# Kernel optimization log

Measured on AMD Instinct MI355X. Metric: run time of the kernel, lower is better.

The kernel has to match this reference:

```python
import jax, jax.numpy as jnp
import numpy as np

EPS = 1e-5  # torch BatchNorm1d default

def _bn(z, g, b):
    # training-mode BatchNorm1d: per-feature batch mean, biased variance
    m = jnp.mean(z, axis=0)
    v = jnp.mean((z - m) ** 2, axis=0)
    return (z - m) * jax.lax.rsqrt(v + EPS) * g + b

def _cell(x, h, c, Wx, Wh, gx, bx, gh, bh):
    gates = _bn(x @ Wx.T, gx, bx) + _bn(h @ Wh.T, gh, bh)  # [B, 4H]
    f, i, o, g = jnp.split(gates, 4, axis=1)  # chunk order f,i,o,g
    c2 = jax.nn.sigmoid(f) * c + jax.nn.sigmoid(i) * jnp.tanh(g)
    h2 = jax.nn.sigmoid(o) * jnp.tanh(c2)
    return h2, c2

def setup_inputs() -> dict:
    key = jax.random.key(0)
    B, H, OUT = 16384, 512, 256
    IN0 = 257  # input_size - 1 (x_dim 256 + y_dim 1)
    ks = jax.random.split(key, 16)
    def lin(k, fo, fi):
        s = 1.0 / np.sqrt(fi)
        return jax.random.uniform(k, (fo, fi), jnp.float32, -s, s)
    return {
        "x": jax.random.normal(ks[0], (B, 256), jnp.float32),
        "y": jax.random.normal(ks[1], (B, 1), jnp.float32),
        "h0": jax.random.normal(ks[2], (2, B, H), jnp.float32),
        "c0": jax.random.normal(ks[3], (2, B, H), jnp.float32),
        "Wx0": lin(ks[4], 4 * H, IN0),
        "Wh0": lin(ks[5], 4 * H, H),
        "gx0": jnp.ones((4 * H,), jnp.float32),
        "bx0": jnp.zeros((4 * H,), jnp.float32),
        "gh0": jnp.ones((4 * H,), jnp.float32),
        "bh0": jnp.zeros((4 * H,), jnp.float32),
        "Wx1": lin(ks[6], 4 * H, H),
        "Wh1": lin(ks[7], 4 * H, H),
        "gx1": jnp.ones((4 * H,), jnp.float32),
        "bx1": jnp.zeros((4 * H,), jnp.float32),
        "gh1": jnp.ones((4 * H,), jnp.float32),
        "bh1": jnp.zeros((4 * H,), jnp.float32),
        "Wo": lin(ks[8], OUT, H),
        "bo": jnp.zeros((OUT,), jnp.float32),
    }

def reference(x, y, h0, c0, Wx0, Wh0, gx0, bx0, gh0, bh0,
              Wx1, Wh1, gx1, bx1, gh1, bh1, Wo, bo):
    inp = jnp.concatenate([x, y], axis=1)  # [B, 257]
    h1, c1 = _cell(inp, h0[0], c0[0], Wx0, Wh0, gx0, bx0, gh0, bh0)
    h2, c2 = _cell(h1, h0[1], c0[1], Wx1, Wh1, gx1, bx1, gh1, bh1)
    out = h2 @ Wo.T + bo  # [B, output_size]
    return (out, jnp.stack([h1, h2]), jnp.stack([c1, c2]))
```

## Files before the change

kernel.cpp:

```cpp
#include <hip/hip_runtime.h>
#include <cstdint>

typedef unsigned short u16;
typedef unsigned int u32;
typedef float floatx4 __attribute__((ext_vector_type(4)));
typedef __bf16 bf16x8 __attribute__((ext_vector_type(8)));
typedef u16 u16x4 __attribute__((ext_vector_type(4)));

__device__ __forceinline__ u16 f2b(float f) {
  u32 u = __builtin_bit_cast(u32, f);
  u32 r = (u + 0x7fffu + ((u >> 16) & 1u)) >> 16;
  return (u16)r;
}
__device__ __forceinline__ float b2f(u16 b) {
  return __builtin_bit_cast(float, (u32)b << 16);
}
__device__ __forceinline__ float sigf(float x) { return 1.f / (1.f + __expf(-x)); }
__device__ __forceinline__ float tanhfast(float x) { return 2.f / (1.f + __expf(-2.f * x)) - 1.f; }

#define GLDS(gp, lp) __builtin_amdgcn_global_load_lds( \
    (const __attribute__((address_space(1))) u32*)(gp), \
    (__attribute__((address_space(3))) u32*)(lp), 16, 0, 0)

template <int KT>
__global__ __launch_bounds__(256) void gemm_p(
    const u16* __restrict__ A, const u16* __restrict__ W, u16* __restrict__ C,
    int N, float* __restrict__ ssum, float* __restrict__ ssq) {
  constexpr int NT = KT / 32;
  __shared__ __align__(16) u16 lds[3 * 8192];

  const int tid = threadIdx.x;
  const int lane = tid & 63;
  const int wid = tid >> 6;
  const int wm = (wid >> 1) << 6;
  const int wn = (wid & 1) << 6;
  const int fr = lane & 15;
  const int fq = lane >> 4;

  const int l = blockIdx.x + (blockIdx.y << 4);
  const int xcd = l & 7;
  const int idx = l >> 3;
  const int bx = idx & 15;
  const int by = (xcd << 4) + (idx >> 4);
  const int m0 = by << 7;
  const int n0 = bx << 7;

  const u16* Ab = A + (size_t)m0 * KT;
  const u16* Wb = W + (size_t)n0 * KT;

  const int ra = tid >> 2;
  const int ca = (tid & 3) ^ ((ra >> 1) & 3);
  const u16* pa0 = Ab + (size_t)ra * KT + ca * 8;
  const u16* pa1 = pa0 + (size_t)64 * KT;
  const u16* pb0 = Wb + (size_t)ra * KT + ca * 8;
  const u16* pb1 = pb0 + (size_t)64 * KT;
  const int da = tid * 8;
  const int db = 4096 + tid * 8;

#define STAGE(kt) do {                                   \
    const int _sl = ((kt) % 3) * 8192;                   \
    const int _ko = (kt) * 32;                           \
    GLDS(pa0 + _ko, &lds[_sl + da]);                     \
    GLDS(pa1 + _ko, &lds[_sl + da + 2048]);              \
    GLDS(pb0 + _ko, &lds[_sl + db]);                     \
    GLDS(pb1 + _ko, &lds[_sl + db + 2048]);              \
  } while (0)

  int aoffs[4], boffs[4];
#pragma unroll
  for (int mf = 0; mf < 4; ++mf) {
    const int R = wm + mf * 16 + fr;
    aoffs[mf] = R * 32 + ((fq ^ ((R >> 1) & 3)) << 3);
  }
#pragma unroll
  for (int nf = 0; nf < 4; ++nf) {
    const int R = wn + nf * 16 + fr;
    boffs[nf] = 4096 + R * 32 + ((fq ^ ((R >> 1) & 3)) << 3);
  }

  floatx4 acc[4][4] = {};

  STAGE(0);
  STAGE(1);

#pragma unroll
  for (int t = 0; t < NT; ++t) {
    if (t == NT - 1) asm volatile("s_waitcnt vmcnt(0)" ::: "memory");
    else             asm volatile("s_waitcnt vmcnt(4)" ::: "memory");
    __builtin_amdgcn_s_barrier();
    __builtin_amdgcn_sched_barrier(0);

    if (t + 2 < NT) STAGE(t + 2);

    const int sl = (t % 3) * 8192;
    bf16x8 bfv[4];
#pragma unroll
    for (int nf = 0; nf < 4; ++nf) bfv[nf] = *(const bf16x8*)&lds[sl + boffs[nf]];
    __builtin_amdgcn_s_setprio(1);
#pragma unroll
    for (int mf = 0; mf < 4; ++mf) {
      const bf16x8 af = *(const bf16x8*)&lds[sl + aoffs[mf]];
#pragma unroll
      for (int nf = 0; nf < 4; ++nf)
        acc[mf][nf] = __builtin_amdgcn_mfma_f32_16x16x32_bf16(af, bfv[nf], acc[mf][nf], 0, 0, 0);
    }
    __builtin_amdgcn_s_setprio(0);
    asm volatile("s_waitcnt lgkmcnt(0)" ::: "memory");
    __builtin_amdgcn_sched_barrier(0);
  }
#undef STAGE

#pragma unroll
  for (int mf = 0; mf < 4; ++mf)
#pragma unroll
    for (int nf = 0; nf < 4; ++nf) {
      const int col = n0 + wn + nf * 16 + fr;
#pragma unroll
      for (int r = 0; r < 4; ++r) {
        const int row = m0 + wm + mf * 16 + fq * 4 + r;
        C[(size_t)row * N + col] = f2b(acc[mf][nf][r]);
      }
    }
#pragma unroll
  for (int nf = 0; nf < 4; ++nf) {
    float s = 0.f, qv = 0.f;
#pragma unroll
    for (int mf = 0; mf < 4; ++mf)
#pragma unroll
      for (int r = 0; r < 4; ++r) {
        const float v = acc[mf][nf][r];
        s += v;
        qv += v * v;
      }
    s += __shfl_xor(s, 16);
    s += __shfl_xor(s, 32);
    qv += __shfl_xor(qv, 16);
    qv += __shfl_xor(qv, 32);
    if (fq == 0) {
      atomicAdd(&ssum[n0 + wn + nf * 16 + fr], s);
      atomicAdd(&ssq[n0 + wn + nf * 16 + fr], qv);
    }
  }
}

template <int STATS, int BIAS>
__global__ __launch_bounds__(256) void gemm_bt(
    const u16* __restrict__ A, const u16* __restrict__ W, void* __restrict__ Cv,
    int N, int K, float* __restrict__ ssum, float* __restrict__ ssq,
    const float* __restrict__ bias) {
  __shared__ u16 As[128 * 32];
  __shared__ u16 Bs[128 * 32];
  const int tid = threadIdx.x;
  const int lane = tid & 63;
  const int wave = tid >> 6;
  const int wm = (wave >> 1) << 6;
  const int wn = (wave & 1) << 6;
  const int m0 = blockIdx.y * 128;
  const int n0 = blockIdx.x * 128;
  const u16* Ab = A + (size_t)m0 * K;
  const u16* Wb = W + (size_t)n0 * K;
  const size_t soff = (size_t)(tid >> 2) * K + ((tid & 3) << 3);
  const size_t soff2 = soff + (size_t)64 * K;
  const int fr = lane & 15;
  const int fq = lane >> 4;
  const int aoff = fr * 32 + fq * 8;

  floatx4 acc[4][4] = {};

  for (int k0 = 0; k0 < K; k0 += 32) {
    __syncthreads();
    GLDS(Ab + soff + k0, &As[tid * 8]);
    GLDS(Ab + soff2 + k0, &As[tid * 8 + 2048]);
    GLDS(Wb + soff + k0, &Bs[tid * 8]);
    GLDS(Wb + soff2 + k0, &Bs[tid * 8 + 2048]);
    __syncthreads();
    bf16x8 af[4], bfv[4];
#pragma unroll
    for (int i = 0; i < 4; ++i) af[i] = *(const bf16x8*)&As[(wm + i * 16) * 32 + aoff];
#pragma unroll
    for (int j = 0; j < 4; ++j) bfv[j] = *(const bf16x8*)&Bs[(wn + j * 16) * 32 + aoff];
#pragma unroll
    for (int i = 0; i < 4; ++i)
#pragma unroll
      for (int j = 0; j < 4; ++j)
        acc[i][j] = __builtin_amdgcn_mfma_f32_16x16x32_bf16(af[i], bfv[j], acc[i][j], 0, 0, 0);
  }

  if (BIAS) {
    float* Cf = (float*)Cv;
#pragma unroll
    for (int i = 0; i < 4; ++i)
#pragma unroll
      for (int j = 0; j < 4; ++j) {
        const int col = n0 + wn + j * 16 + fr;
        const float bv = bias[col];
#pragma unroll
        for (int r = 0; r < 4; ++r) {
          const int row = m0 + wm + i * 16 + fq * 4 + r;
          Cf[(size_t)row * N + col] = acc[i][j][r] + bv;
        }
      }
  } else {
    u16* Cb = (u16*)Cv;
#pragma unroll
    for (int i = 0; i < 4; ++i)
#pragma unroll
      for (int j = 0; j < 4; ++j) {
        const int col = n0 + wn + j * 16 + fr;
#pragma unroll
        for (int r = 0; r < 4; ++r) {
          const int row = m0 + wm + i * 16 + fq * 4 + r;
          Cb[(size_t)row * N + col] = f2b(acc[i][j][r]);
        }
      }
  }

  if (STATS) {
#pragma unroll
    for (int j = 0; j < 4; ++j) {
      float s = 0.f, q = 0.f;
#pragma unroll
      for (int i = 0; i < 4; ++i)
#pragma unroll
        for (int r = 0; r < 4; ++r) {
          const float v = acc[i][j][r];
          s += v;
          q += v * v;
        }
      s += __shfl_xor(s, 16);
      s += __shfl_xor(s, 32);
      q += __shfl_xor(q, 16);
      q += __shfl_xor(q, 32);
      if (fq == 0) {
        atomicAdd(&ssum[n0 + wn + j * 16 + fr], s);
        atomicAdd(&ssq[n0 + wn + j * 16 + fr], q);
      }
    }
  }
}

__global__ void pad_inp_k(const float* __restrict__ x, const float* __restrict__ y,
                          u16* __restrict__ o) {
  const int idx = blockIdx.x * 256 + threadIdx.x;
  const int b = idx / 288;
  const int c = idx - b * 288;
  float v = 0.f;
  if (c < 256) v = x[b * 256 + c];
  else if (c == 256) v = y[b];
  o[idx] = f2b(v);
}

__global__ void pad_w_k(const float* __restrict__ w, u16* __restrict__ o) {
  const int idx = blockIdx.x * 256 + threadIdx.x;
  const int r = idx / 288;
  const int c = idx - r * 288;
  o[idx] = f2b(c < 257 ? w[r * 257 + c] : 0.f);
}

__global__ void f2b_k(const float4* __restrict__ in, u16x4* __restrict__ o, int n4) {
  const int idx = blockIdx.x * 256 + threadIdx.x;
  if (idx < n4) {
    const float4 v = in[idx];
    u16x4 r;
    r.x = f2b(v.x);
    r.y = f2b(v.y);
    r.z = f2b(v.z);
    r.w = f2b(v.w);
    o[idx] = r;
  }
}

__global__ void coef_k(const float* __restrict__ st, const float* __restrict__ gx,
                       const float* __restrict__ bx, const float* __restrict__ gh,
                       const float* __restrict__ bh, float* __restrict__ cf, float invB) {
  const int j = blockIdx.x * 256 + threadIdx.x;
  const float mx = st[j] * invB;
  const float vx = st[2048 + j] * invB - mx * mx;
  const float ax = gx[j] * rsqrtf(vx + 1e-5f);
  const float mh = st[4096 + j] * invB;
  const float vh = st[6144 + j] * invB - mh * mh;
  const float ah = gh[j] * rsqrtf(vh + 1e-5f);
  cf[j] = ax;
  cf[2048 + j] = ah;
  cf[4096 + j] = bx[j] - mx * ax + bh[j] - mh * ah;
}

__global__ void cell_k(const u16* __restrict__ Zx, const u16* __restrict__ Zh,
                       const float* __restrict__ coef, const float* __restrict__ cin,
                       float* __restrict__ hout, float* __restrict__ cout,
                       u16* __restrict__ hb) {
  const int idx = blockIdx.x * 256 + threadIdx.x;
  const int b = idx >> 8;
  const int j2 = (idx & 255) << 1;
  const size_t rb = (size_t)b << 11;
  float gv[4][2];
#pragma unroll
  for (int g = 0; g < 4; ++g) {
    const int col = (g << 9) + j2;
    const u32 zx = *(const u32*)(Zx + rb + col);
    const u32 zh = *(const u32*)(Zh + rb + col);
#pragma unroll
    for (int t = 0; t < 2; ++t) {
      const float zxv = b2f((u16)(zx >> (16 * t)));
      const float zhv = b2f((u16)(zh >> (16 * t)));
      gv[g][t] = coef[col + t] * zxv + coef[2048 + col + t] * zhv + coef[4096 + col + t];
    }
  }
  const size_t ob = ((size_t)b << 9) + j2;
  const float2 cp = *(const float2*)(cin + ob);
  float cn[2], hn[2];
#pragma unroll
  for (int t = 0; t < 2; ++t) {
    const float cprev = t ? cp.y : cp.x;
    const float cc = sigf(gv[0][t]) * cprev + sigf(gv[1][t]) * tanhfast(gv[3][t]);
    cn[t] = cc;
    hn[t] = sigf(gv[2][t]) * tanhfast(cc);
  }
  *(float2*)(cout + ob) = make_float2(cn[0], cn[1]);
  *(float2*)(hout + ob) = make_float2(hn[0], hn[1]);
  *(u32*)(hb + ob) = (u32)f2b(hn[0]) | ((u32)f2b(hn[1]) << 16);
}

extern "C" void kernel_launch(void* const* d_in, const int* in_sizes, int n_in,
                              void* d_out, int out_size, void* d_ws, size_t ws_size,
                              hipStream_t stream) {
  (void)in_sizes; (void)n_in; (void)out_size; (void)ws_size;
  constexpr int B = 16384, H = 512, G = 2048, KP = 288, K1 = 512, NOUT = 256;

  const float* x = (const float*)d_in[0];
  const float* y = (const float*)d_in[1];
  const float* h0 = (const float*)d_in[2];
  const float* c0 = (const float*)d_in[3];
  const float* Wx0 = (const float*)d_in[4];
  const float* Wh0 = (const float*)d_in[5];
  const float* gx0 = (const float*)d_in[6];
  const float* bx0 = (const float*)d_in[7];
  const float* gh0 = (const float*)d_in[8];
  const float* bh0 = (const float*)d_in[9];
  const float* Wx1 = (const float*)d_in[10];
  const float* Wh1 = (const float*)d_in[11];
  const float* gx1 = (const float*)d_in[12];
  const float* bx1 = (const float*)d_in[13];
  const float* gh1 = (const float*)d_in[14];
  const float* bh1 = (const float*)d_in[15];
  const float* Wo = (const float*)d_in[16];
  const float* bo = (const float*)d_in[17];

  char* p = (char*)d_ws;
  u16* Zx = (u16*)p;   p += (size_t)B * G * 2;
  u16* Zh = (u16*)p;   p += (size_t)B * G * 2;
  u16* h0b = (u16*)p;  p += (size_t)2 * B * H * 2;
  u16* h1b = (u16*)p;  p += (size_t)B * H * 2;
  u16* inpb = (u16*)p; p += (size_t)B * KP * 2;
  u16* wx0b = (u16*)p; p += (size_t)G * KP * 2;
  u16* wh0b = (u16*)p; p += (size_t)G * K1 * 2;
  u16* wx1b = (u16*)p; p += (size_t)G * K1 * 2;
  u16* wh1b = (u16*)p; p += (size_t)G * K1 * 2;
  u16* wob = (u16*)p;  p += (size_t)NOUT * K1 * 2;
  float* stats = (float*)p; p += (size_t)8 * G * 4;
  float* coef = (float*)p;  p += (size_t)6 * G * 4;

  float* out_o = (float*)d_out;
  float* h_o = out_o + (size_t)B * NOUT;
  float* c_o = h_o + (size_t)2 * B * H;

  hipMemsetAsync(stats, 0, (size_t)8 * G * sizeof(float), stream);

  pad_inp_k<<<B * KP / 256, 256, 0, stream>>>(x, y, inpb);
  pad_w_k<<<G * KP / 256, 256, 0, stream>>>(Wx0, wx0b);
  f2b_k<<<2 * B * H / 4 / 256, 256, 0, stream>>>((const float4*)h0, (u16x4*)h0b, 2 * B * H / 4);
  f2b_k<<<G * K1 / 4 / 256, 256, 0, stream>>>((const float4*)Wh0, (u16x4*)wh0b, G * K1 / 4);
  f2b_k<<<G * K1 / 4 / 256, 256, 0, stream>>>((const float4*)Wx1, (u16x4*)wx1b, G * K1 / 4);
  f2b_k<<<G * K1 / 4 / 256, 256, 0, stream>>>((const float4*)Wh1, (u16x4*)wh1b, G * K1 / 4);
  f2b_k<<<NOUT * K1 / 4 / 256, 256, 0, stream>>>((const float4*)Wo, (u16x4*)wob, NOUT * K1 / 4);

  const dim3 blk(256);
  const dim3 gbig(G / 128, B / 128);

  gemm_p<KP><<<gbig, blk, 0, stream>>>(inpb, wx0b, Zx, G, stats + 0 * G, stats + 1 * G);
  gemm_p<K1><<<gbig, blk, 0, stream>>>(h0b, wh0b, Zh, G, stats + 2 * G, stats + 3 * G);
  coef_k<<<G / 256, 256, 0, stream>>>(stats, gx0, bx0, gh0, bh0, coef, 1.f / B);
  cell_k<<<B, 256, 0, stream>>>(Zx, Zh, coef, c0, h_o, c_o, h1b);

  gemm_p<K1><<<gbig, blk, 0, stream>>>(h1b, wx1b, Zx, G, stats + 4 * G, stats + 5 * G);
  gemm_p<K1><<<gbig, blk, 0, stream>>>(h0b + (size_t)B * H, wh1b, Zh, G, stats + 6 * G, stats + 7 * G);
  coef_k<<<G / 256, 256, 0, stream>>>(stats + 4 * G, gx1, bx1, gh1, bh1, coef + 3 * G, 1.f / B);
  cell_k<<<B, 256, 0, stream>>>(Zx, Zh, coef + 3 * G, c0 + (size_t)B * H,
                                h_o + (size_t)B * H, c_o + (size_t)B * H, h1b);

  const dim3 gout(NOUT / 128, B / 128);
  gemm_bt<0, 1><<<gout, blk, 0, stream>>>(h1b, wob, out_o, NOUT, K1, nullptr, nullptr, bo);
}
```

Measured before the change: 600.8 us.

## Store GEMM outputs as row-pair packed bf16 and merge paired GEMMs and prep kernels

The gate GEMMs now write their bf16 outputs as u32 words holding two adjacent rows at the same column, packed with v_cvt_pk_bf16_f32. The cell kernel is rewritten to read this interleaved layout and process two batch rows per thread. The x- and h-GEMMs of each layer are launched together as one grid with a z dimension, and the many conversion and padding kernels are merged into two launches. The aim is to replace narrow 2-byte scattered stores with 4-byte ones and to cut launch count and tail idle time. The cost is that the intermediate Z layout is now non-standard and every reader must use the matching indexing.

```diff
diff --git a/kernel.cpp b/kernel.cpp
--- a/kernel.cpp
+++ b/kernel.cpp
@@ -15,6 +15,11 @@
 __device__ __forceinline__ float b2f(u16 b) {
   return __builtin_bit_cast(float, (u32)b << 16);
 }
+__device__ __forceinline__ u32 pkbf(float lo, float hi) {
+  u32 r;
+  asm("v_cvt_pk_bf16_f32 %0, %1, %2" : "=v"(r) : "v"(lo), "v"(hi));
+  return r;
+}
 __device__ __forceinline__ float sigf(float x) { return 1.f / (1.f + __expf(-x)); }
 __device__ __forceinline__ float tanhfast(float x) { return 2.f / (1.f + __expf(-2.f * x)) - 1.f; }
 
@@ -23,12 +28,10 @@
     (__attribute__((address_space(3))) u32*)(lp), 16, 0, 0)
 
 template <int KT>
-__global__ __launch_bounds__(256) void gemm_p(
-    const u16* __restrict__ A, const u16* __restrict__ W, u16* __restrict__ C,
-    int N, float* __restrict__ ssum, float* __restrict__ ssq) {
+__device__ __forceinline__ void gemm_body(
+    const u16* __restrict__ A, const u16* __restrict__ W, u32* __restrict__ C32,
+    int N, float* __restrict__ ssum, float* __restrict__ ssq, u16* lds) {
   constexpr int NT = KT / 32;
-  __shared__ __align__(16) u16 lds[3 * 8192];
-
   const int tid = threadIdx.x;
   const int lane = tid & 63;
   const int wid = tid >> 6;
@@ -111,16 +114,16 @@
 #undef STAGE
 
 #pragma unroll
-  for (int mf = 0; mf < 4; ++mf)
+  for (int mf = 0; mf < 4; ++mf) {
+    const int rp = (m0 + wm + mf * 16 + fq * 4) >> 1;
 #pragma unroll
     for (int nf = 0; nf < 4; ++nf) {
       const int col = n0 + wn + nf * 16 + fr;
 #pragma unroll
-      for (int r = 0; r < 4; ++r) {
-        const int row = m0 + wm + mf * 16 + fq * 4 + r;
-        C[(size_t)row * N + col] = f2b(acc[mf][nf][r]);
-      }
-    }
+      for (int p = 0; p < 2; ++p)
+        C32[(size_t)(rp + p) * N + col] = pkbf(acc[mf][nf][2 * p], acc[mf][nf][2 * p + 1]);
+    }
+  }
 #pragma unroll
   for (int nf = 0; nf < 4; ++nf) {
     float s = 0.f, qv = 0.f;
@@ -143,11 +146,20 @@
   }
 }
 
-template <int STATS, int BIAS>
-__global__ __launch_bounds__(256) void gemm_bt(
-    const u16* __restrict__ A, const u16* __restrict__ W, void* __restrict__ Cv,
-    int N, int K, float* __restrict__ ssum, float* __restrict__ ssq,
-    const float* __restrict__ bias) {
+template <int KTX, int KTH>
+__global__ __launch_bounds__(256) void gemm_pair(
+    const u16* __restrict__ Ax, const u16* __restrict__ Wx, u32* __restrict__ Cx,
+    float* __restrict__ ssx, float* __restrict__ sqx,
+    const u16* __restrict__ Ah, const u16* __restrict__ Wh, u32* __restrict__ Ch,
+    float* __restrict__ ssh, float* __restrict__ sqh, int N) {
+  __shared__ __align__(16) u16 lds[3 * 8192];
+  if (blockIdx.z == 0) gemm_body<KTX>(Ax, Wx, Cx, N, ssx, sqx, lds);
+  else                 gemm_body<KTH>(Ah, Wh, Ch, N, ssh, sqh, lds);
+}
+
+__global__ __launch_bounds__(256) void gemm_out(
+    const u16* __restrict__ A, const u16* __restrict__ W, float* __restrict__ C,
+    int N, int K, const float* __restrict__ bias) {
   __shared__ u16 As[128 * 32];
   __shared__ u16 Bs[128 * 32];
   const int tid = threadIdx.x;
@@ -186,88 +198,74 @@
         acc[i][j] = __builtin_amdgcn_mfma_f32_16x16x32_bf16(af[i], bfv[j], acc[i][j], 0, 0, 0);
   }
 
-  if (BIAS) {
-    float* Cf = (float*)Cv;
-#pragma unroll
-    for (int i = 0; i < 4; ++i)
-#pragma unroll
-      for (int j = 0; j < 4; ++j) {
-        const int col = n0 + wn + j * 16 + fr;
-        const float bv = bias[col];
-#pragma unroll
-        for (int r = 0; r < 4; ++r) {
-          const int row = m0 + wm + i * 16 + fq * 4 + r;
-          Cf[(size_t)row * N + col] = acc[i][j][r] + bv;
-        }
+#pragma unroll
+  for (int i = 0; i < 4; ++i)
+#pragma unroll
+    for (int j = 0; j < 4; ++j) {
+      const int col = n0 + wn + j * 16 + fr;
+      const float bv = bias[col];
+#pragma unroll
+      for (int r = 0; r < 4; ++r) {
+        const int row = m0 + wm + i * 16 + fq * 4 + r;
+        C[(size_t)row * N + col] = acc[i][j][r] + bv;
       }
+    }
+}
+
+__global__ void prep_inputs_k(const float* __restrict__ x, const float* __restrict__ y,
+                              u16* __restrict__ inpb,
+                              const float4* __restrict__ h0, u16x4* __restrict__ h0b) {
+  const int bid = blockIdx.x;
+  if (bid < 4608) {
+    const int idx = bid * 256 + threadIdx.x;
+    const int b = idx / 72;
+    const int c4 = idx - b * 72;
+    float4 v = make_float4(0.f, 0.f, 0.f, 0.f);
+    if (c4 < 64) v = ((const float4*)x)[b * 64 + c4];
+    else if (c4 == 64) v.x = y[b];
+    u16x4 r;
+    r.x = f2b(v.x); r.y = f2b(v.y); r.z = f2b(v.z); r.w = f2b(v.w);
+    *(u16x4*)&inpb[b * 288 + c4 * 4] = r;
   } else {
-    u16* Cb = (u16*)Cv;
-#pragma unroll
-    for (int i = 0; i < 4; ++i)
-#pragma unroll
-      for (int j = 0; j < 4; ++j) {
-        const int col = n0 + wn + j * 16 + fr;
-#pragma unroll
-        for (int r = 0; r < 4; ++r) {
-          const int row = m0 + wm + i * 16 + fq * 4 + r;
-          Cb[(size_t)row * N + col] = f2b(acc[i][j][r]);
-        }
-      }
-  }
-
-  if (STATS) {
-#pragma unroll
-    for (int j = 0; j < 4; ++j) {
-      float s = 0.f, q = 0.f;
-#pragma unroll
-      for (int i = 0; i < 4; ++i)
-#pragma unroll
-        for (int r = 0; r < 4; ++r) {
-          const float v = acc[i][j][r];
-          s += v;
-          q += v * v;
-        }
-      s += __shfl_xor(s, 16);
-      s += __shfl_xor(s, 32);
-      q += __shfl_xor(q, 16);
-      q += __shfl_xor(q, 32);
-      if (fq == 0) {
-        atomicAdd(&ssum[n0 + wn + j * 16 + fr], s);
-        atomicAdd(&ssq[n0 + wn + j * 16 + fr], q);
-      }
-    }
-  }
-}
-
-__global__ void pad_inp_k(const float* __restrict__ x, const float* __restrict__ y,
-                          u16* __restrict__ o) {
-  const int idx = blockIdx.x * 256 + threadIdx.x;
-  const int b = idx / 288;
-  const int c = idx - b * 288;
-  float v = 0.f;
-  if (c < 256) v = x[b * 256 + c];
-  else if (c == 256) v = y[b];
-  o[idx] = f2b(v);
-}
-
-__global__ void pad_w_k(const float* __restrict__ w, u16* __restrict__ o) {
-  const int idx = blockIdx.x * 256 + threadIdx.x;
-  const int r = idx / 288;
-  const int c = idx - r * 288;
-  o[idx] = f2b(c < 257 ? w[r * 257 + c] : 0.f);
-}
-
-__global__ void f2b_k(const float4* __restrict__ in, u16x4* __restrict__ o, int n4) {
-  const int idx = blockIdx.x * 256 + threadIdx.x;
-  if (idx < n4) {
-    const float4 v = in[idx];
+    const int idx = (bid - 4608) * 256 + threadIdx.x;
+    const float4 v = h0[idx];
     u16x4 r;
-    r.x = f2b(v.x);
-    r.y = f2b(v.y);
-    r.z = f2b(v.z);
-    r.w = f2b(v.w);
-    o[idx] = r;
-  }
+    r.x = f2b(v.x); r.y = f2b(v.y); r.z = f2b(v.z); r.w = f2b(v.w);
+    h0b[idx] = r;
+  }
+}
+
+__global__ void prep_weights_k(
+    const float* __restrict__ Wx0, u16* __restrict__ wx0b,
+    const float4* __restrict__ Wh0, u16x4* __restrict__ wh0b,
+    const float4* __restrict__ Wx1, u16x4* __restrict__ wx1b,
+    const float4* __restrict__ Wh1, u16x4* __restrict__ wh1b,
+    const float4* __restrict__ Wo, u16x4* __restrict__ wob) {
+  const int bid = blockIdx.x;
+  if (bid < 2304) {
+    const int idx = bid * 256 + threadIdx.x;
+    const int r = idx / 288;
+    const int c = idx - r * 288;
+    wx0b[idx] = f2b(c < 257 ? Wx0[r * 257 + c] : 0.f);
+    return;
+  }
+  const float4* src;
+  u16x4* dst;
+  int idx;
+  if (bid < 2304 + 3072) {
+    const int seg = (bid - 2304) >> 10;
+    idx = ((bid - 2304) & 1023) * 256 + threadIdx.x;
+    src = seg == 0 ? Wh0 : (seg == 1 ? Wx1 : Wh1);
+    dst = seg == 0 ? wh0b : (seg == 1 ? wx1b : wh1b);
+  } else {
+    idx = (bid - 2304 - 3072) * 256 + threadIdx.x;
+    src = Wo;
+    dst = wob;
+  }
+  const float4 v = src[idx];
+  u16x4 r;
+  r.x = f2b(v.x); r.y = f2b(v.y); r.z = f2b(v.z); r.w = f2b(v.w);
+  dst[idx] = r;
 }
 
 __global__ void coef_k(const float* __restrict__ st, const float* __restrict__ gx,
@@ -285,40 +283,45 @@
   cf[4096 + j] = bx[j] - mx * ax + bh[j] - mh * ah;
 }
 
-__global__ void cell_k(const u16* __restrict__ Zx, const u16* __restrict__ Zh,
-                       const float* __restrict__ coef, const float* __restrict__ cin,
-                       float* __restrict__ hout, float* __restrict__ cout,
-                       u16* __restrict__ hb) {
+__global__ __launch_bounds__(256) void cell2_k(
+    const u32* __restrict__ Zx, const u32* __restrict__ Zh,
+    const float* __restrict__ coef, const float* __restrict__ cin,
+    float* __restrict__ hout, float* __restrict__ cout, u16* __restrict__ hb) {
   const int idx = blockIdx.x * 256 + threadIdx.x;
-  const int b = idx >> 8;
+  const int bp = idx >> 8;
   const int j2 = (idx & 255) << 1;
-  const size_t rb = (size_t)b << 11;
-  float gv[4][2];
+  const size_t zb = (size_t)bp << 11;
+  float gv[4][2][2];
 #pragma unroll
   for (int g = 0; g < 4; ++g) {
     const int col = (g << 9) + j2;
-    const u32 zx = *(const u32*)(Zx + rb + col);
-    const u32 zh = *(const u32*)(Zh + rb + col);
+    const uint2 zx2 = *(const uint2*)&Zx[zb + col];
+    const uint2 zh2 = *(const uint2*)&Zh[zb + col];
+    const float2 ax = *(const float2*)&coef[col];
+    const float2 ah = *(const float2*)&coef[2048 + col];
+    const float2 cb = *(const float2*)&coef[4096 + col];
+    gv[g][0][0] = ax.x * b2f((u16)zx2.x) + ah.x * b2f((u16)zh2.x) + cb.x;
+    gv[g][1][0] = ax.x * b2f((u16)(zx2.x >> 16)) + ah.x * b2f((u16)(zh2.x >> 16)) + cb.x;
+    gv[g][0][1] = ax.y * b2f((u16)zx2.y) + ah.y * b2f((u16)zh2.y) + cb.y;
+    gv[g][1][1] = ax.y * b2f((u16)(zx2.y >> 16)) + ah.y * b2f((u16)(zh2.y >> 16)) + cb.y;
+  }
+#pragma unroll
+  for (int s = 0; s < 2; ++s) {
+    const int b = (bp << 1) + s;
+    const size_t ob = ((size_t)b << 9) + j2;
+    const float2 cp = *(const float2*)(cin + ob);
+    float cn[2], hn[2];
 #pragma unroll
     for (int t = 0; t < 2; ++t) {
-      const float zxv = b2f((u16)(zx >> (16 * t)));
-      const float zhv = b2f((u16)(zh >> (16 * t)));
-      gv[g][t] = coef[col + t] * zxv + coef[2048 + col + t] * zhv + coef[4096 + col + t];
-    }
-  }
-  const size_t ob = ((size_t)b << 9) + j2;
-  const float2 cp = *(const float2*)(cin + ob);
-  float cn[2], hn[2];
-#pragma unroll
-  for (int t = 0; t < 2; ++t) {
-    const float cprev = t ? cp.y : cp.x;
-    const float cc = sigf(gv[0][t]) * cprev + sigf(gv[1][t]) * tanhfast(gv[3][t]);
-    cn[t] = cc;
-    hn[t] = sigf(gv[2][t]) * tanhfast(cc);
-  }
-  *(float2*)(cout + ob) = make_float2(cn[0], cn[1]);
-  *(float2*)(hout + ob) = make_float2(hn[0], hn[1]);
-  *(u32*)(hb + ob) = (u32)f2b(hn[0]) | ((u32)f2b(hn[1]) << 16);
+      const float cprev = t ? cp.y : cp.x;
+      const float cc = sigf(gv[0][s][t]) * cprev + sigf(gv[1][s][t]) * tanhfast(gv[3][s][t]);
+      cn[t] = cc;
+      hn[t] = sigf(gv[2][s][t]) * tanhfast(cc);
+    }
+    *(float2*)(cout + ob) = make_float2(cn[0], cn[1]);
+    *(float2*)(hout + ob) = make_float2(hn[0], hn[1]);
+    *(u32*)(hb + ob) = pkbf(hn[0], hn[1]);
+  }
 }
 
 extern "C" void kernel_launch(void* const* d_in, const int* in_sizes, int n_in,
@@ -366,28 +369,28 @@
 
   hipMemsetAsync(stats, 0, (size_t)8 * G * sizeof(float), stream);
 
-  pad_inp_k<<<B * KP / 256, 256, 0, stream>>>(x, y, inpb);
-  pad_w_k<<<G * KP / 256, 256, 0, stream>>>(Wx0, wx0b);
-  f2b_k<<<2 * B * H / 4 / 256, 256, 0, stream>>>((const float4*)h0, (u16x4*)h0b, 2 * B * H / 4);
-  f2b_k<<<G * K1 / 4 / 256, 256, 0, stream>>>((const float4*)Wh0, (u16x4*)wh0b, G * K1 / 4);
-  f2b_k<<<G * K1 / 4 / 256, 256, 0, stream>>>((const float4*)Wx1, (u16x4*)wx1b, G * K1 / 4);
-  f2b_k<<<G * K1 / 4 / 256, 256, 0, stream>>>((const float4*)Wh1, (u16x4*)wh1b, G * K1 / 4);
-  f2b_k<<<NOUT * K1 / 4 / 256, 256, 0, stream>>>((const float4*)Wo, (u16x4*)wob, NOUT * K1 / 4);
+  prep_inputs_k<<<4608 + 16384, 256, 0, stream>>>(x, y, inpb, (const float4*)h0, (u16x4*)h0b);
+  prep_weights_k<<<2304 + 3072 + 128, 256, 0, stream>>>(
+      Wx0, wx0b, (const float4*)Wh0, (u16x4*)wh0b, (const float4*)Wx1, (u16x4*)wx1b,
+      (const float4*)Wh1, (u16x4*)wh1b, (const float4*)Wo, (u16x4*)wob);
 
   const dim3 blk(256);
-  const dim3 gbig(G / 128, B / 128);
-
-  gemm_p<KP><<<gbig, blk, 0, stream>>>(inpb, wx0b, Zx, G, stats + 0 * G, stats + 1 * G);
-  gemm_p<K1><<<gbig, blk, 0, stream>>>(h0b, wh0b, Zh, G, stats + 2 * G, stats + 3 * G);
+  const dim3 gpair(G / 128, B / 128, 2);
+
+  gemm_pair<KP, K1><<<gpair, blk, 0, stream>>>(
+      inpb, wx0b, (u32*)Zx, stats + 0 * G, stats + 1 * G,
+      h0b, wh0b, (u32*)Zh, stats + 2 * G, stats + 3 * G, G);
   coef_k<<<G / 256, 256, 0, stream>>>(stats, gx0, bx0, gh0, bh0, coef, 1.f / B);
-  cell_k<<<B, 256, 0, stream>>>(Zx, Zh, coef, c0, h_o, c_o, h1b);
-
-  gemm_p<K1><<<gbig, blk, 0, stream>>>(h1b, wx1b, Zx, G, stats + 4 * G, stats + 5 * G);
-  gemm_p<K1><<<gbig, blk, 0, stream>>>(h0b + (size_t)B * H, wh1b, Zh, G, stats + 6 * G, stats + 7 * G);
+  cell2_k<<<B / 2, 256, 0, stream>>>((const u32*)Zx, (const u32*)Zh, coef, c0, h_o, c_o, h1b);
+
+  gemm_pair<K1, K1><<<gpair, blk, 0, stream>>>(
+      h1b, wx1b, (u32*)Zx, stats + 4 * G, stats + 5 * G,
+      h0b + (size_t)B * H, wh1b, (u32*)Zh, stats + 6 * G, stats + 7 * G, G);
   coef_k<<<G / 256, 256, 0, stream>>>(stats + 4 * G, gx1, bx1, gh1, bh1, coef + 3 * G, 1.f / B);
-  cell_k<<<B, 256, 0, stream>>>(Zx, Zh, coef + 3 * G, c0 + (size_t)B * H,
-                                h_o + (size_t)B * H, c_o + (size_t)B * H, h1b);
+  cell2_k<<<B / 2, 256, 0, stream>>>((const u32*)Zx, (const u32*)Zh, coef + 3 * G,
+                                     c0 + (size_t)B * H, h_o + (size_t)B * H,
+                                     c_o + (size_t)B * H, h1b);
 
   const dim3 gout(NOUT / 128, B / 128);
-  gemm_bt<0, 1><<<gout, blk, 0, stream>>>(h1b, wob, out_o, NOUT, K1, nullptr, nullptr, bo);
-}
+  gemm_out<<<gout, blk, 0, stream>>>(h1b, wob, out_o, NOUT, K1, bo);
+}
```

New measurement: 540.5 us. 10.0% less time.
